# Kernel tuning notes

Hardware: AMD Instinct MI355X
Metric: run time of the kernel (lower is better)

## Reference

```python
import jax, jax.numpy as jnp
import numpy as np

N_NODES = 50000
N_EDGES = 800000
HIDDEN = 128
OUT = 128


def setup_inputs() -> dict:
    key = jax.random.key(0)
    k1, k2, k3, k4, k5, k6 = jax.random.split(key, 6)
    h = jax.random.normal(k1, (N_NODES, HIDDEN), dtype=jnp.float32)
    src = jax.random.randint(k2, (N_EDGES,), 0, N_NODES, dtype=jnp.int64)
    dst = jax.random.randint(k3, (N_EDGES,), 0, N_NODES, dtype=jnp.int64)
    scale = 1.0 / np.sqrt(HIDDEN)
    W_edge = jax.random.normal(k4, (OUT, HIDDEN), dtype=jnp.float32) * scale
    W_self = jax.random.normal(k5, (OUT, HIDDEN), dtype=jnp.float32) * scale
    b_self = jax.random.normal(k6, (OUT,), dtype=jnp.float32) * scale
    return {"h": h, "src": src, "dst": dst, "W_edge": W_edge, "W_self": W_self, "b_self": b_self}


def reference(h, src, dst, W_edge, W_self, b_self):
    n = h.shape[0]
    # edge_transform(src_features): same linear on every edge -> transform nodes once, then gather
    msg_node = h @ W_edge.T                       # [N, OUT]
    msg = msg_node[src]                           # [E, OUT] gather
    sums = jax.ops.segment_sum(msg, dst, num_segments=n)  # [N, OUT] scatter-add
    deg = jax.ops.segment_sum(jnp.ones((dst.shape[0],), dtype=h.dtype), dst, num_segments=n)
    h1 = sums / jnp.maximum(deg, 1.0)[:, None]    # mean; zero in-degree -> 0 (DGL semantics)
    out = jax.nn.relu(h @ W_self.T + b_self + h1)
    return out
```

## Files before the change

kernel.cpp:

```cpp
#include <hip/hip_runtime.h>

#define N_HID 128
#define CAP   64
#define OVF_CAP 8192
#define NSLICE 8
#define PBLK   256

typedef short bf16x8 __attribute__((ext_vector_type(8)));
typedef float f32x4  __attribute__((ext_vector_type(4)));

static __device__ __forceinline__ unsigned short f2bf(float f)
{
    unsigned int u = __float_as_uint(f);
    u = (u + 0x7fffu + ((u >> 16) & 1u)) >> 16;
    return (unsigned short)u;
}
static __device__ __forceinline__ float bf2f(unsigned int bits16)
{
    return __uint_as_float(bits16 << 16);
}

__global__ __launch_bounds__(256) void fragmentize(
    const float* __restrict__ h,
    const float* __restrict__ We,
    const float* __restrict__ Ws,
    unsigned short* __restrict__ Ah,
    unsigned short* __restrict__ Be,
    unsigned short* __restrict__ Bs,
    int n, int nrt)
{
    int b = blockIdx.x;
    const float* src; unsigned short* dstF; int rt, nrows;
    if (b < nrt)          { src = h;  dstF = Ah; rt = b;           nrows = n;   }
    else if (b < nrt + 8) { src = We; dstF = Be; rt = b - nrt;     nrows = 128; }
    else                  { src = Ws; dstF = Bs; rt = b - nrt - 8; nrows = 128; }

    int t  = threadIdx.x;
    int kc = t >> 6;
    int l  = t & 63;
    int m  = l & 15;
    int q  = l >> 4;

    int row = rt * 16 + m;
    if (row > nrows - 1) row = nrows - 1;

    const float* p = &src[(size_t)row * N_HID + kc * 32 + q * 8];
    float4 v0 = *(const float4*)p;
    float4 v1 = *(const float4*)(p + 4);

    uint4 pk;
    pk.x = (unsigned int)f2bf(v0.x) | ((unsigned int)f2bf(v0.y) << 16);
    pk.y = (unsigned int)f2bf(v0.z) | ((unsigned int)f2bf(v0.w) << 16);
    pk.z = (unsigned int)f2bf(v1.x) | ((unsigned int)f2bf(v1.y) << 16);
    pk.w = (unsigned int)f2bf(v1.z) | ((unsigned int)f2bf(v1.w) << 16);

    *(uint4*)&dstF[(size_t)rt * 2048 + kc * 512 + l * 8] = pk;
}

__global__ __launch_bounds__(256) void gemm_mfma2(
    const unsigned short* __restrict__ Afrag,
    const unsigned short* __restrict__ Be,
    const unsigned short* __restrict__ Bsf,
    const float* __restrict__ bias,
    unsigned short* __restrict__ msgOut,
    float* __restrict__ fOut,
    int n, int nrt, int nwb)
{
    int b    = blockIdx.x;
    bool sp  = b >= nwb;
    int bl   = sp ? b - nwb : b;
    int w    = bl * 4 + ((int)threadIdx.x >> 6);
    if (w >= nrt) return;
    int l = threadIdx.x & 63;

    const unsigned short* Bfrag = sp ? Bsf : Be;

    const bf16x8* Ap = (const bf16x8*)(Afrag + (size_t)w * 2048);
    bf16x8 a0 = Ap[l], a1 = Ap[64 + l], a2 = Ap[128 + l], a3 = Ap[192 + l];

    const int m0   = w * 16;
    const int colb = l & 15;
    const int rq   = (l >> 4) * 4;

#pragma unroll
    for (int ct = 0; ct < 8; ++ct) {
        const bf16x8* Bp = (const bf16x8*)(Bfrag + (size_t)ct * 2048);
        f32x4 acc = {0.f, 0.f, 0.f, 0.f};
        acc = __builtin_amdgcn_mfma_f32_16x16x32_bf16(a0, Bp[l],       acc, 0, 0, 0);
        acc = __builtin_amdgcn_mfma_f32_16x16x32_bf16(a1, Bp[64 + l],  acc, 0, 0, 0);
        acc = __builtin_amdgcn_mfma_f32_16x16x32_bf16(a2, Bp[128 + l], acc, 0, 0, 0);
        acc = __builtin_amdgcn_mfma_f32_16x16x32_bf16(a3, Bp[192 + l], acc, 0, 0, 0);

        int col = ct * 16 + colb;
        if (sp) {
            float bv = bias[col];
#pragma unroll
            for (int r = 0; r < 4; ++r) {
                int row = m0 + rq + r;
                if (row < n) fOut[(size_t)row * N_HID + col] = acc[r] + bv;
            }
        } else {
#pragma unroll
            for (int r = 0; r < 4; ++r) {
                int row = m0 + rq + r;
                if (row < n) msgOut[(size_t)row * N_HID + col] = f2bf(acc[r]);
            }
        }
    }
}

__global__ __launch_bounds__(256) void part_count(
    const int* __restrict__ dst, int* __restrict__ blockCnt, int E, int n)
{
    int t = threadIdx.x, b = blockIdx.x;
    int c[NSLICE];
#pragma unroll
    for (int s = 0; s < NSLICE; ++s) c[s] = 0;

    for (int e = b * 256 + t; e < E; e += PBLK * 256) {
        int sl = (int)(((long long)dst[e] * NSLICE) / n);
#pragma unroll
        for (int s = 0; s < NSLICE; ++s) c[s] += (sl == s);
    }

    __shared__ int red[NSLICE * 4];
    int lane = t & 63, wid = t >> 6;
#pragma unroll
    for (int s = 0; s < NSLICE; ++s) {
        int v = c[s];
#pragma unroll
        for (int off = 32; off; off >>= 1) v += __shfl_down(v, off);
        if (lane == 0) red[s * 4 + wid] = v;
    }
    __syncthreads();
    if (t < NSLICE)
        blockCnt[t * PBLK + b] = red[t*4+0] + red[t*4+1] + red[t*4+2] + red[t*4+3];
}

__global__ __launch_bounds__(256) void part_scan(
    const int* __restrict__ blockCnt, int* __restrict__ blockBase,
    int* __restrict__ sbase, int E)
{
    __shared__ int ws[4];
    int t = threadIdx.x, lane = t & 63, wid = t >> 6;
    int v[8]; int s = 0;
#pragma unroll
    for (int i = 0; i < 8; ++i) { v[i] = blockCnt[t * 8 + i]; s += v[i]; }
    int val = s;
#pragma unroll
    for (int off = 1; off < 64; off <<= 1) {
        int y = __shfl_up(val, off);
        if (lane >= off) val += y;
    }
    if (lane == 63) ws[wid] = val;
    __syncthreads();
    if (t == 0) { int a = 0; for (int w = 0; w < 4; ++w) { int tmp = ws[w]; ws[w] = a; a += tmp; } }
    __syncthreads();
    int excl = ws[wid] + val - s;
#pragma unroll
    for (int i = 0; i < 8; ++i) { int tv = v[i]; blockBase[t * 8 + i] = excl; excl += tv; }
    __syncthreads();
    if (t < NSLICE) sbase[t] = blockBase[t * PBLK];
    if (t == 0)     sbase[NSLICE] = E;
}

__global__ __launch_bounds__(256) void part_scatter(
    const int* __restrict__ src, const int* __restrict__ dst,
    const int* __restrict__ blockBase, unsigned int* __restrict__ part,
    int E, int n)
{
    __shared__ int cur[NSLICE];
    int t = threadIdx.x, b = blockIdx.x;
    if (t < NSLICE) cur[t] = blockBase[t * PBLK + b];
    __syncthreads();
    for (int e = b * 256 + t; e < E; e += PBLK * 256) {
        int d = dst[e], s = src[e];
        int sl  = (int)(((long long)d * NSLICE) / n);
        int pos = atomicAdd(&cur[sl], 1);
        part[pos] = ((unsigned int)d << 16) | (unsigned int)s;
    }
}

__global__ __launch_bounds__(256) void bucket_scatter2(
    const unsigned int* __restrict__ part,
    const int* __restrict__ sbase,
    int* __restrict__ cnt,
    int* __restrict__ bucket,
    int* __restrict__ ovfn,
    long long* __restrict__ ovf)
{
    const int slice = blockIdx.x & 7;
    const int g     = blockIdx.x >> 3;
    const int nG    = (int)(gridDim.x >> 3);
    const int lo    = sbase[slice];
    const int hi    = sbase[slice + 1];
    const int m     = hi - lo;

    const int chunk = (m + nG - 1) / nG;
    const int e0 = lo + g * chunk;
    int e1 = e0 + chunk; if (e1 > hi) e1 = hi;

    for (int e = e0 + (int)threadIdx.x; e < e1; e += 256) {
        unsigned int pk = part[e];
        int d = (int)(pk >> 16);
        int s = (int)(pk & 0xffffu);
        int c = atomicAdd(&cnt[d], 1);
        if (c < CAP) {
            bucket[(size_t)d * CAP + c] = s;
        } else {
            int o = atomicAdd(ovfn, 1);
            if (o < OVF_CAP) ovf[o] = ((long long)d << 32) | (unsigned int)s;
        }
    }
}

__global__ __launch_bounds__(256) void gather_finish(
    const int* __restrict__ cnt,
    const int* __restrict__ bucket,
    const int* __restrict__ ovfn,
    const long long* __restrict__ ovf,
    const unsigned short* __restrict__ msg,
    float* __restrict__ out,
    int n)
{
    int node = blockIdx.x * 4 + (threadIdx.x >> 6);
    if (node >= n) return;
    int lane = threadIdx.x & 63;
    int deg  = cnt[node];
    int m    = deg < CAP ? deg : CAP;

    const int* bk = &bucket[(size_t)node * CAP];
    const unsigned int* m32 = (const unsigned int*)msg;

    float ax = 0.f, ay = 0.f;
    int i = 0;
    for (; i + 4 <= m; i += 4) {
        int s0 = bk[i + 0], s1 = bk[i + 1], s2 = bk[i + 2], s3 = bk[i + 3];
        unsigned int v0 = m32[(size_t)s0 * 64 + lane];
        unsigned int v1 = m32[(size_t)s1 * 64 + lane];
        unsigned int v2 = m32[(size_t)s2 * 64 + lane];
        unsigned int v3 = m32[(size_t)s3 * 64 + lane];
        ax += bf2f(v0 & 0xffffu) + bf2f(v1 & 0xffffu) + bf2f(v2 & 0xffffu) + bf2f(v3 & 0xffffu);
        ay += bf2f(v0 >> 16)     + bf2f(v1 >> 16)     + bf2f(v2 >> 16)     + bf2f(v3 >> 16);
    }
    for (; i < m; ++i) {
        unsigned int v = m32[(size_t)bk[i] * 64 + lane];
        ax += bf2f(v & 0xffffu);
        ay += bf2f(v >> 16);
    }

    if (deg > CAP) {
        int no = *ovfn; if (no > OVF_CAP) no = OVF_CAP;
        for (int o = 0; o < no; ++o) {
            long long pk = ovf[o];
            if ((int)(pk >> 32) == node) {
                unsigned int v = m32[(size_t)(unsigned int)pk * 64 + lane];
                ax += bf2f(v & 0xffffu);
                ay += bf2f(v >> 16);
            }
        }
    }

    float sc = deg > 0 ? 1.0f / (float)deg : 0.f;

    float2* o2 = (float2*)out;
    float2 sv  = o2[(size_t)node * 64 + lane];
    float2 r;
    r.x = fmaxf(sv.x + ax * sc, 0.f);
    r.y = fmaxf(sv.y + ay * sc, 0.f);
    o2[(size_t)node * 64 + lane] = r;
}

extern "C" void kernel_launch(void* const* d_in, const int* in_sizes, int n_in,
                              void* d_out, int out_size, void* d_ws, size_t ws_size,
                              hipStream_t stream)
{
    const float* h   = (const float*)d_in[0];
    const int*   src = (const int*)d_in[1];
    const int*   dst = (const int*)d_in[2];
    const float* We  = (const float*)d_in[3];
    const float* Ws  = (const float*)d_in[4];
    const float* bs  = (const float*)d_in[5];
    float*       out = (float*)d_out;

    const int n   = in_sizes[0] / N_HID;
    const int E   = in_sizes[1];
    const int nrt = (n + 15) / 16;
    const int nwb = (nrt + 3) / 4;

    unsigned short* msg = (unsigned short*)d_ws;
    unsigned short* Ah  = msg + (size_t)n * N_HID;
    int*            bucket = (int*)Ah;
    unsigned short* Be  = Ah + (size_t)nrt * 2048;
    unsigned short* Bs  = Be + 8 * 2048;
    int*  cnt  = (int*)(Bs + 8 * 2048);
    int*  ovfn = cnt + n;
    long long* ovf = (long long*)(ovfn + 8);
    int*  blockCnt  = (int*)(ovf + OVF_CAP);
    int*  blockBase = blockCnt + PBLK * NSLICE;
    int*  sbase     = blockBase + PBLK * NSLICE;
    unsigned int* part = (unsigned int*)(sbase + 16);

    hipMemsetAsync(cnt, 0, sizeof(int) * (size_t)(n + 8), stream);

    part_count<<<PBLK, 256, 0, stream>>>(dst, blockCnt, E, n);
    part_scan<<<1, 256, 0, stream>>>(blockCnt, blockBase, sbase, E);
    part_scatter<<<PBLK, 256, 0, stream>>>(src, dst, blockBase, part, E, n);

    fragmentize<<<nrt + 16, 256, 0, stream>>>(h, We, Ws, Ah, Be, Bs, n, nrt);
    gemm_mfma2<<<2 * nwb, 256, 0, stream>>>(Ah, Be, Bs, bs, msg, out, n, nrt, nwb);

    bucket_scatter2<<<512, 256, 0, stream>>>(part, sbase, cnt, bucket, ovfn, ovf);
    gather_finish<<<(n + 3) / 4, 256, 0, stream>>>(cnt, bucket, ovfn, ovf, msg, out, n);
}
```

Baseline: 196.2 us.

## Fuse h fragmentization into GEMM and fold memset and weight prep into existing kernels

Removes the separate fragmentize kernel and the bf16 copy of h. The GEMM now loads fp32 h tiles into LDS, converts them to bf16 MFMA fragments in registers, and computes both the edge and self products in one block. The cnt memset is moved into part_count, and weight fragmentization is folded into the scan kernel as extra blocks. This cuts kernel launches and a round trip of h through global memory, at the cost of LDS use and less parallelism per block, since one block now does two passes instead of two separate blocks.

```diff
diff --git a/kernel.cpp b/kernel.cpp
--- a/kernel.cpp
+++ b/kernel.cpp
@@ -5,6 +5,7 @@
 #define OVF_CAP 8192
 #define NSLICE 8
 #define PBLK   256
+#define LDW   132
 
 typedef short bf16x8 __attribute__((ext_vector_type(8)));
 typedef float f32x4  __attribute__((ext_vector_type(4)));
@@ -15,104 +16,24 @@
     u = (u + 0x7fffu + ((u >> 16) & 1u)) >> 16;
     return (unsigned short)u;
 }
+static __device__ __forceinline__ unsigned int pack2(float a, float b)
+{
+    return (unsigned int)f2bf(a) | ((unsigned int)f2bf(b) << 16);
+}
 static __device__ __forceinline__ float bf2f(unsigned int bits16)
 {
     return __uint_as_float(bits16 << 16);
 }
 
-__global__ __launch_bounds__(256) void fragmentize(
-    const float* __restrict__ h,
-    const float* __restrict__ We,
-    const float* __restrict__ Ws,
-    unsigned short* __restrict__ Ah,
-    unsigned short* __restrict__ Be,
-    unsigned short* __restrict__ Bs,
-    int n, int nrt)
-{
-    int b = blockIdx.x;
-    const float* src; unsigned short* dstF; int rt, nrows;
-    if (b < nrt)          { src = h;  dstF = Ah; rt = b;           nrows = n;   }
-    else if (b < nrt + 8) { src = We; dstF = Be; rt = b - nrt;     nrows = 128; }
-    else                  { src = Ws; dstF = Bs; rt = b - nrt - 8; nrows = 128; }
-
-    int t  = threadIdx.x;
-    int kc = t >> 6;
-    int l  = t & 63;
-    int m  = l & 15;
-    int q  = l >> 4;
-
-    int row = rt * 16 + m;
-    if (row > nrows - 1) row = nrows - 1;
-
-    const float* p = &src[(size_t)row * N_HID + kc * 32 + q * 8];
-    float4 v0 = *(const float4*)p;
-    float4 v1 = *(const float4*)(p + 4);
-
-    uint4 pk;
-    pk.x = (unsigned int)f2bf(v0.x) | ((unsigned int)f2bf(v0.y) << 16);
-    pk.y = (unsigned int)f2bf(v0.z) | ((unsigned int)f2bf(v0.w) << 16);
-    pk.z = (unsigned int)f2bf(v1.x) | ((unsigned int)f2bf(v1.y) << 16);
-    pk.w = (unsigned int)f2bf(v1.z) | ((unsigned int)f2bf(v1.w) << 16);
-
-    *(uint4*)&dstF[(size_t)rt * 2048 + kc * 512 + l * 8] = pk;
-}
-
-__global__ __launch_bounds__(256) void gemm_mfma2(
-    const unsigned short* __restrict__ Afrag,
-    const unsigned short* __restrict__ Be,
-    const unsigned short* __restrict__ Bsf,
-    const float* __restrict__ bias,
-    unsigned short* __restrict__ msgOut,
-    float* __restrict__ fOut,
-    int n, int nrt, int nwb)
-{
-    int b    = blockIdx.x;
-    bool sp  = b >= nwb;
-    int bl   = sp ? b - nwb : b;
-    int w    = bl * 4 + ((int)threadIdx.x >> 6);
-    if (w >= nrt) return;
-    int l = threadIdx.x & 63;
-
-    const unsigned short* Bfrag = sp ? Bsf : Be;
-
-    const bf16x8* Ap = (const bf16x8*)(Afrag + (size_t)w * 2048);
-    bf16x8 a0 = Ap[l], a1 = Ap[64 + l], a2 = Ap[128 + l], a3 = Ap[192 + l];
-
-    const int m0   = w * 16;
-    const int colb = l & 15;
-    const int rq   = (l >> 4) * 4;
-
-#pragma unroll
-    for (int ct = 0; ct < 8; ++ct) {
-        const bf16x8* Bp = (const bf16x8*)(Bfrag + (size_t)ct * 2048);
-        f32x4 acc = {0.f, 0.f, 0.f, 0.f};
-        acc = __builtin_amdgcn_mfma_f32_16x16x32_bf16(a0, Bp[l],       acc, 0, 0, 0);
-        acc = __builtin_amdgcn_mfma_f32_16x16x32_bf16(a1, Bp[64 + l],  acc, 0, 0, 0);
-        acc = __builtin_amdgcn_mfma_f32_16x16x32_bf16(a2, Bp[128 + l], acc, 0, 0, 0);
-        acc = __builtin_amdgcn_mfma_f32_16x16x32_bf16(a3, Bp[192 + l], acc, 0, 0, 0);
-
-        int col = ct * 16 + colb;
-        if (sp) {
-            float bv = bias[col];
-#pragma unroll
-            for (int r = 0; r < 4; ++r) {
-                int row = m0 + rq + r;
-                if (row < n) fOut[(size_t)row * N_HID + col] = acc[r] + bv;
-            }
-        } else {
-#pragma unroll
-            for (int r = 0; r < 4; ++r) {
-                int row = m0 + rq + r;
-                if (row < n) msgOut[(size_t)row * N_HID + col] = f2bf(acc[r]);
-            }
-        }
-    }
-}
-
 __global__ __launch_bounds__(256) void part_count(
-    const int* __restrict__ dst, int* __restrict__ blockCnt, int E, int n)
+    const int* __restrict__ dst, int* __restrict__ blockCnt,
+    int* __restrict__ cnt, int* __restrict__ ovfn, int E, int n)
 {
     int t = threadIdx.x, b = blockIdx.x;
+
+    for (int i = b * 256 + t; i < n; i += PBLK * 256) cnt[i] = 0;
+    if (b == 0 && t == 0) *ovfn = 0;
+
     int c[NSLICE];
 #pragma unroll
     for (int s = 0; s < NSLICE; ++s) c[s] = 0;
@@ -137,31 +58,52 @@
         blockCnt[t * PBLK + b] = red[t*4+0] + red[t*4+1] + red[t*4+2] + red[t*4+3];
 }
 
-__global__ __launch_bounds__(256) void part_scan(
+__global__ __launch_bounds__(256) void scan_fragw(
     const int* __restrict__ blockCnt, int* __restrict__ blockBase,
-    int* __restrict__ sbase, int E)
-{
-    __shared__ int ws[4];
-    int t = threadIdx.x, lane = t & 63, wid = t >> 6;
-    int v[8]; int s = 0;
-#pragma unroll
-    for (int i = 0; i < 8; ++i) { v[i] = blockCnt[t * 8 + i]; s += v[i]; }
-    int val = s;
-#pragma unroll
-    for (int off = 1; off < 64; off <<= 1) {
-        int y = __shfl_up(val, off);
-        if (lane >= off) val += y;
-    }
-    if (lane == 63) ws[wid] = val;
-    __syncthreads();
-    if (t == 0) { int a = 0; for (int w = 0; w < 4; ++w) { int tmp = ws[w]; ws[w] = a; a += tmp; } }
-    __syncthreads();
-    int excl = ws[wid] + val - s;
-#pragma unroll
-    for (int i = 0; i < 8; ++i) { int tv = v[i]; blockBase[t * 8 + i] = excl; excl += tv; }
-    __syncthreads();
-    if (t < NSLICE) sbase[t] = blockBase[t * PBLK];
-    if (t == 0)     sbase[NSLICE] = E;
+    int* __restrict__ sbase, int E,
+    const float* __restrict__ We, const float* __restrict__ Ws,
+    unsigned short* __restrict__ Be, unsigned short* __restrict__ Bs)
+{
+    int t = threadIdx.x, b = blockIdx.x;
+    if (b == 0) {
+        __shared__ int wsm[4];
+        int lane = t & 63, wid = t >> 6;
+        int v[8]; int s = 0;
+#pragma unroll
+        for (int i = 0; i < 8; ++i) { v[i] = blockCnt[t * 8 + i]; s += v[i]; }
+        int val = s;
+#pragma unroll
+        for (int off = 1; off < 64; off <<= 1) {
+            int y = __shfl_up(val, off);
+            if (lane >= off) val += y;
+        }
+        if (lane == 63) wsm[wid] = val;
+        __syncthreads();
+        if (t == 0) { int a = 0; for (int w = 0; w < 4; ++w) { int tmp = wsm[w]; wsm[w] = a; a += tmp; } }
+        __syncthreads();
+        int excl = wsm[wid] + val - s;
+#pragma unroll
+        for (int i = 0; i < 8; ++i) { int tv = v[i]; blockBase[t * 8 + i] = excl; excl += tv; }
+        __syncthreads();
+        if (t < NSLICE) sbase[t] = blockBase[t * PBLK];
+        if (t == 0)     sbase[NSLICE] = E;
+    } else {
+        int bb = b - 1;
+        const float* src = (bb < 8) ? We : Ws;
+        unsigned short* dstF = (bb < 8) ? Be : Bs;
+        int rt = bb & 7;
+
+        int kc = t >> 6, l = t & 63, m = l & 15, q = l >> 4;
+        const float* p = &src[(size_t)(rt * 16 + m) * N_HID + kc * 32 + q * 8];
+        float4 v0 = *(const float4*)p;
+        float4 v1 = *(const float4*)(p + 4);
+        uint4 pk;
+        pk.x = pack2(v0.x, v0.y);
+        pk.y = pack2(v0.z, v0.w);
+        pk.z = pack2(v1.x, v1.y);
+        pk.w = pack2(v1.z, v1.w);
+        *(uint4*)&dstF[(size_t)rt * 2048 + kc * 512 + l * 8] = pk;
+    }
 }
 
 __global__ __launch_bounds__(256) void part_scatter(
@@ -178,6 +120,84 @@
         int sl  = (int)(((long long)d * NSLICE) / n);
         int pos = atomicAdd(&cur[sl], 1);
         part[pos] = ((unsigned int)d << 16) | (unsigned int)s;
+    }
+}
+
+__global__ __launch_bounds__(256) void gemm_fused(
+    const float* __restrict__ h,
+    const unsigned short* __restrict__ Be,
+    const unsigned short* __restrict__ Bsf,
+    const float* __restrict__ bias,
+    unsigned short* __restrict__ msgOut,
+    float* __restrict__ fOut,
+    int n, int nrt)
+{
+    __shared__ float As[4][16 * LDW];
+
+    int t = threadIdx.x;
+    int w = t >> 6, l = t & 63;
+    int rt = blockIdx.x * 4 + w;
+    bool active = rt < nrt;
+    int rtc = active ? rt : nrt - 1;
+    int row0 = rtc * 16;
+
+    float* A = As[w];
+#pragma unroll
+    for (int it = 0; it < 8; ++it) {
+        int f  = it * 64 + l;
+        int r  = f >> 5;
+        int c4 = (f & 31) * 4;
+        int gr = row0 + r; if (gr > n - 1) gr = n - 1;
+        *(float4*)&A[r * LDW + c4] = *(const float4*)&h[(size_t)gr * N_HID + c4];
+    }
+    __syncthreads();
+
+    int m = l & 15, q = l >> 4;
+    union { uint4 u; bf16x8 v; } af[4];
+#pragma unroll
+    for (int kc = 0; kc < 4; ++kc) {
+        const float* p = &A[m * LDW + kc * 32 + q * 8];
+        float4 v0 = *(const float4*)p;
+        float4 v1 = *(const float4*)(p + 4);
+        af[kc].u.x = pack2(v0.x, v0.y);
+        af[kc].u.y = pack2(v0.z, v0.w);
+        af[kc].u.z = pack2(v1.x, v1.y);
+        af[kc].u.w = pack2(v1.z, v1.w);
+    }
+
+    const int colb = l & 15;
+    const int rq   = (l >> 4) * 4;
+
+#pragma unroll 1
+    for (int pass = 0; pass < 2; ++pass) {
+        const unsigned short* Bfrag = pass ? Bsf : Be;
+#pragma unroll
+        for (int ct = 0; ct < 8; ++ct) {
+            const bf16x8* Bp = (const bf16x8*)(Bfrag + (size_t)ct * 2048);
+            f32x4 acc = {0.f, 0.f, 0.f, 0.f};
+            acc = __builtin_amdgcn_mfma_f32_16x16x32_bf16(af[0].v, Bp[l],       acc, 0, 0, 0);
+            acc = __builtin_amdgcn_mfma_f32_16x16x32_bf16(af[1].v, Bp[64 + l],  acc, 0, 0, 0);
+            acc = __builtin_amdgcn_mfma_f32_16x16x32_bf16(af[2].v, Bp[128 + l], acc, 0, 0, 0);
+            acc = __builtin_amdgcn_mfma_f32_16x16x32_bf16(af[3].v, Bp[192 + l], acc, 0, 0, 0);
+
+            if (active) {
+                int col = ct * 16 + colb;
+                if (pass) {
+                    float bv = bias[col];
+#pragma unroll
+                    for (int r = 0; r < 4; ++r) {
+                        int row = row0 + rq + r;
+                        if (row < n) fOut[(size_t)row * N_HID + col] = acc[r] + bv;
+                    }
+                } else {
+#pragma unroll
+                    for (int r = 0; r < 4; ++r) {
+                        int row = row0 + rq + r;
+                        if (row < n) msgOut[(size_t)row * N_HID + col] = f2bf(acc[r]);
+                    }
+                }
+            }
+        }
     }
 }
 
@@ -286,12 +306,10 @@
     const int n   = in_sizes[0] / N_HID;
     const int E   = in_sizes[1];
     const int nrt = (n + 15) / 16;
-    const int nwb = (nrt + 3) / 4;
 
     unsigned short* msg = (unsigned short*)d_ws;
-    unsigned short* Ah  = msg + (size_t)n * N_HID;
-    int*            bucket = (int*)Ah;
-    unsigned short* Be  = Ah + (size_t)nrt * 2048;
+    int*   bucket = (int*)(msg + (size_t)n * N_HID);
+    unsigned short* Be  = (unsigned short*)(bucket + (size_t)n * CAP);
     unsigned short* Bs  = Be + 8 * 2048;
     int*  cnt  = (int*)(Bs + 8 * 2048);
     int*  ovfn = cnt + n;
@@ -301,15 +319,10 @@
     int*  sbase     = blockBase + PBLK * NSLICE;
     unsigned int* part = (unsigned int*)(sbase + 16);
 
-    hipMemsetAsync(cnt, 0, sizeof(int) * (size_t)(n + 8), stream);
-
-    part_count<<<PBLK, 256, 0, stream>>>(dst, blockCnt, E, n);
-    part_scan<<<1, 256, 0, stream>>>(blockCnt, blockBase, sbase, E);
+    part_count<<<PBLK, 256, 0, stream>>>(dst, blockCnt, cnt, ovfn, E, n);
+    scan_fragw<<<17, 256, 0, stream>>>(blockCnt, blockBase, sbase, E, We, Ws, Be, Bs);
     part_scatter<<<PBLK, 256, 0, stream>>>(src, dst, blockBase, part, E, n);
-
-    fragmentize<<<nrt + 16, 256, 0, stream>>>(h, We, Ws, Ah, Be, Bs, n, nrt);
-    gemm_mfma2<<<2 * nwb, 256, 0, stream>>>(Ah, Be, Bs, bs, msg, out, n, nrt, nwb);
-
+    gemm_fused<<<(nrt + 3) / 4, 256, 0, stream>>>(h, Be, Bs, bs, msg, out, n, nrt);
     bucket_scatter2<<<512, 256, 0, stream>>>(part, sbase, cnt, bucket, ovfn, ovf);
     gather_finish<<<(n + 3) / 4, 256, 0, stream>>>(cnt, bucket, ovfn, ovf, msg, out, n);
 }
```

Measured after the change: 193.0 us. No clear change (-1.6%).
